# Kernel tuning notes

Hardware: AMD Instinct MI355X
Metric: run time of the kernel (lower is better)

## Reference

```python
import jax, jax.numpy as jnp
import numpy as np

B, C, H, W = 1, 256, 48, 64
HW = H * W
HIDDEN, CTX = 128, 64
LEVELS, RADIUS = 4, 4
WIN = 2 * RADIUS + 1
P = WIN * WIN                     # 81 lookup points per level
CORR_DIM = P * LEVELS             # 324
TOP_K = 3
ITERS = 4
STEP_ROT, STEP_TRANS = 0.02, 0.02


def _sample_templates():
    # 12 directions x 3 scales + identity = 37 pose perturbations (as in __init__)
    base = [([0,0,0],[1,0,0]),([0,0,0],[-1,0,0]),([0,0,0],[0,1,0]),([0,0,0],[0,-1,0]),
            ([0,0,0],[0,0,1]),([0,0,0],[0,0,-1]),([1,0,0],[0,0,0]),([-1,0,0],[0,0,0]),
            ([0,1,0],[0,0,0]),([0,-1,0],[0,0,0]),([0,0,1],[0,0,0]),([0,0,-1],[0,0,0])]
    scales = np.array([0.25, 1.0, 4.0], np.float32)
    rot = np.repeat(np.array([r for r, _ in base], np.float32), 3, axis=0)
    trs = np.repeat(np.array([t for _, t in base], np.float32), 3, axis=0)
    sc = np.tile(scales, 12)
    axes = rot / np.clip(np.linalg.norm(rot, axis=1, keepdims=True), 1e-8, None)
    ha = STEP_ROT * sc / 2.0
    dq = np.stack([np.cos(ha), axes[:, 0]*np.sin(ha), axes[:, 1]*np.sin(ha), axes[:, 2]*np.sin(ha)], -1)
    dt = trs * (STEP_TRANS * sc[:, None])
    dq = np.concatenate([dq, [[1., 0., 0., 0.]]], 0)
    dt = np.concatenate([dt, [[0., 0., 0.]]], 0)
    return jnp.asarray(dq), jnp.asarray(dt)

DQ, DT = _sample_templates()     # (37,4), (37,3)
N_SAMPLES = DQ.shape[0]


def qmul(q, r):
    w1, x1, y1, z1 = jnp.moveaxis(q, -1, 0)
    w2, x2, y2, z2 = jnp.moveaxis(r, -1, 0)
    return jnp.stack([w1*w2 - x1*x2 - y1*y2 - z1*z2,
                      w1*x2 + x1*w2 + y1*z2 - z1*y2,
                      w1*y2 - x1*z2 + y1*w2 + z1*x2,
                      w1*z2 + x1*y2 - y1*x2 + z1*w2], -1)


def qapply(q, v):
    qv = jnp.concatenate([jnp.zeros(v.shape[:-1] + (1,), v.dtype), v], -1)
    qc = q * jnp.array([1., -1., -1., -1.], q.dtype)
    return qmul(qmul(q, qv), qc)[..., 1:]


def quat_to_R(q):
    w, x, y, z = jnp.moveaxis(q, -1, 0)
    R = jnp.stack([1-2*(y*y+z*z), 2*(x*y-w*z), 2*(x*z+w*y),
                   2*(x*y+w*z), 1-2*(x*x+z*z), 2*(y*z-w*x),
                   2*(x*z-w*y), 2*(y*z+w*x), 1-2*(x*x+y*y)], -1)
    return R.reshape(q.shape[:-1] + (3, 3))


def conv3(x, w, b):
    y = jax.lax.conv_general_dilated(x, w, (1, 1), 'SAME',
                                     dimension_numbers=('NCHW', 'OIHW', 'NCHW'))
    return y + b[None, :, None, None]


def bilinear_lookup(corr_flat, Hl, Wl, x, y):
    # corr_flat: (B,HW,Hl*Wl); x,y: (B,N,HW,P) -> (B,N,HW,P), zero padding outside
    x0 = jnp.floor(x)
    y0 = jnp.floor(y)
    out = jnp.zeros(x.shape, corr_flat.dtype)
    def gather(idx):
        g = lambda ix: jnp.take_along_axis(corr_flat, ix, axis=-1)
        return jax.vmap(g, in_axes=1, out_axes=1)(idx)   # vmap over N, no corr copy
    for dx_, dy_ in ((0, 0), (1, 0), (0, 1), (1, 1)):
        xi = x0 + dx_
        yi = y0 + dy_
        wgt = (1 - jnp.abs(x - xi)) * (1 - jnp.abs(y - yi))
        valid = (xi >= 0) & (xi < Wl) & (yi >= 0) & (yi < Hl)
        idx = (jnp.clip(yi, 0, Hl - 1) * Wl + jnp.clip(xi, 0, Wl - 1)).astype(jnp.int32)
        out = out + jnp.where(valid, wgt, 0.0) * gather(idx)
    return out


def _forward(fmap_rgb, fmap_depth, depth, context, intrinsics,
             Wz, bz, Wr, br, Wq, bq, Wh, bh, Wfc, bfc):
    f32 = jnp.float32
    fx = 60. + 40. * intrinsics[:, 0]
    fy = 60. + 40. * intrinsics[:, 1]
    cx = W / 2. + 4. * (intrinsics[:, 2] - 0.5)
    cy = H / 2. + 4. * (intrinsics[:, 3] - 0.5)
    d = 4.0 + 20.0 * depth                                  # (B,H,W) metric depth

    # 4D correlation pyramid: corr[b,i,:,:] = <fmap_depth pixel i, fmap_rgb>
    fd = fmap_depth.reshape(B, C, HW).transpose(0, 2, 1)    # (B,HW,C)
    corr = jnp.einsum('bic,bchw->bihw', fd, fmap_rgb) / jnp.sqrt(f32(C))
    pyramid = []
    cl, Hl, Wl = corr, H, W
    for _ in range(LEVELS):
        pyramid.append((cl.reshape(B, HW, Hl * Wl), Hl, Wl))
        cl = cl.reshape(B, HW, Hl // 2, 2, Wl // 2, 2).mean(axis=(3, 5))
        Hl //= 2
        Wl //= 2

    # back-projected depth points (B,HW,3)
    vv, uu = jnp.meshgrid(jnp.arange(H, dtype=f32), jnp.arange(W, dtype=f32), indexing='ij')
    uu = uu.reshape(HW)
    vv = vv.reshape(HW)
    df = d.reshape(B, HW)
    X = jnp.stack([(uu[None] - cx[:, None]) / fx[:, None] * df,
                   (vv[None] - cy[:, None]) / fy[:, None] * df, df], -1)

    off = jnp.arange(-RADIUS, RADIUS + 1, dtype=f32)
    oy, ox = jnp.meshgrid(off, off, indexing='ij')
    ox = ox.reshape(P)
    oy = oy.reshape(P)

    pose = jnp.tile(jnp.array([1., 0., 0., 0., 0., 0., 0.], f32)[None, :], (B, 1))
    h = jnp.zeros((B, HIDDEN, H, W), f32)

    for _ in range(ITERS):
        qc, tc = pose[:, :4], pose[:, 4:7]
        quats = qmul(qc[:, None, :], DQ[None])              # (B,N,4)
        quats = quats / jnp.linalg.norm(quats, axis=-1, keepdims=True)
        trans = tc[:, None, :] + qapply(qc[:, None, :], DT[None])
        Rm = quat_to_R(quats)                               # (B,N,3,3)
        Xc = jnp.einsum('bnij,bpj->bnpi', Rm, X) + trans[:, :, None, :]
        z = jnp.clip(Xc[..., 2], 0.1, None)
        u = fx[:, None, None] * Xc[..., 0] / z + cx[:, None, None]   # (B,N,HW)
        v = fy[:, None, None] * Xc[..., 1] / z + cy[:, None, None]
        feats = []
        for lvl, (cfl, Hl_, Wl_) in enumerate(pyramid):
            s = f32(2 ** lvl)
            xl = u[..., None] / s + ox
            yl = v[..., None] / s + oy
            feats.append(bilinear_lookup(cfl, Hl_, Wl_, xl, yl))
        cf = jnp.concatenate(feats, -1)                     # (B,N,HW,CORR_DIM)
        conf = cf.mean(axis=(2, 3))                         # (B,N) sample confidence
        topv, topi = jax.lax.top_k(conf, TOP_K)
        wk = jax.nn.softmax(topv, axis=-1)                  # confidence-weighted top-K
        idx = jnp.broadcast_to(topi[:, :, None, None], (B, TOP_K, HW, CORR_DIM))
        sel = jnp.take_along_axis(cf, idx, axis=1)
        fused = (wk[:, :, None, None] * sel).sum(1)         # (B,HW,CORR_DIM)
        fused = fused.transpose(0, 2, 1).reshape(B, CORR_DIM, H, W)

        # ConvGRU update
        x_in = jnp.concatenate([fused, context], 1)
        hx = jnp.concatenate([h, x_in], 1)
        zg = jax.nn.sigmoid(conv3(hx, Wz, bz))
        rg = jax.nn.sigmoid(conv3(hx, Wr, br))
        qg = jnp.tanh(conv3(jnp.concatenate([rg * h, x_in], 1), Wq, bq))
        h = (1 - zg) * h + zg * qg

        # 7D pose delta head + quaternion/Lie-style update
        feat = jax.nn.relu(conv3(h, Wh, bh)).mean(axis=(2, 3))
        delta = 0.01 * (feat @ Wfc + bfc)                   # (B,7)
        dq = jnp.concatenate([1.0 + delta[:, :1], delta[:, 1:4]], -1)
        dq = dq / jnp.linalg.norm(dq, axis=-1, keepdims=True)
        tn = tc + qapply(qc, delta[:, 4:7])
        qn = qmul(qc, dq)
        qn = qn / jnp.linalg.norm(qn, axis=-1, keepdims=True)
        pose = jnp.concatenate([qn, tn], -1)
    return pose


def setup_inputs() -> dict:
    key = jax.random.key(0)
    ks = jax.random.split(key, 12)
    rn = lambda k, shape, s=1.0: s * jax.random.normal(k, shape, jnp.float32)
    Gin = HIDDEN + CORR_DIM + CTX
    sc = 1.0 / np.sqrt(Gin * 9)
    sh = 1.0 / np.sqrt(HIDDEN * 9)
    return {
        'fmap_rgb': rn(ks[0], (B, C, H, W)),
        'fmap_depth': rn(ks[1], (B, C, H, W)),
        'depth': jax.random.uniform(ks[2], (B, H, W), jnp.float32),
        'context': rn(ks[3], (B, CTX, H, W)),
        'intrinsics': jax.random.uniform(ks[4], (B, 4), jnp.float32),
        'Wz': rn(ks[5], (HIDDEN, Gin, 3, 3), sc), 'bz': jnp.zeros((HIDDEN,), jnp.float32),
        'Wr': rn(ks[6], (HIDDEN, Gin, 3, 3), sc), 'br': jnp.zeros((HIDDEN,), jnp.float32),
        'Wq': rn(ks[7], (HIDDEN, Gin, 3, 3), sc), 'bq': jnp.zeros((HIDDEN,), jnp.float32),
        'Wh': rn(ks[8], (HIDDEN, HIDDEN, 3, 3), sh), 'bh': jnp.zeros((HIDDEN,), jnp.float32),
        'Wfc': rn(ks[9], (HIDDEN, 7), 1.0 / np.sqrt(HIDDEN)), 'bfc': jnp.zeros((7,), jnp.float32),
    }


def reference(fmap_rgb, fmap_depth, depth, context, intrinsics,
              Wz, bz, Wr, br, Wq, bq, Wh, bh, Wfc, bfc):
    return _forward(fmap_rgb, fmap_depth, depth, context, intrinsics,
                    Wz, bz, Wr, br, Wq, bq, Wh, bh, Wfc, bfc)
```

## Files before the change

### kernel.cpp

```cpp
#include <hip/hip_runtime.h>
#include <math.h>

constexpr int kH = 48, kW = 64, kHW = 3072, kC = 256;
constexpr int kHidden = 128, kCtx = 64;
constexpr int kP = 81, kCorrDim = 324;
constexpr int kNS = 37, kIters = 4;
constexpr int kGin = kHidden + kCorrDim + kCtx;
constexpr int kWp2 = 66, kHp2 = 50, kPix = 3300;
constexpr int kCF = 416;
constexpr int kCHh = 128;

constexpr int kSB0 = 0, kSB1 = 4292, kSB2 = 5720, kSB3 = 6292, kSBTot = 6580;
constexpr int kHB0 = 0, kHB1 = 3552, kHB2 = 4560, kHB3 = 4872, kHBTot = 4980;

constexpr size_t U_CORR0 = 0;
constexpr size_t U_CORR1 = U_CORR0 + (size_t)kHW * 3072;
constexpr size_t U_CORR2 = U_CORR1 + (size_t)kHW * 768;
constexpr size_t U_CORR3 = U_CORR2 + (size_t)kHW * 192;
constexpr size_t U_END0  = U_CORR3 + (size_t)kHW * 48;
constexpr size_t F_X     = U_END0 / 2;
constexpr size_t F_H     = F_X + (size_t)kHW * 3;
constexpr size_t F_ZPRE  = F_H + (size_t)kHidden * kHW;
constexpr size_t F_END1  = F_ZPRE + (size_t)kHidden * kHW;
constexpr size_t U_FCT   = F_END1 * 2;
constexpr size_t U_HT    = U_FCT + (size_t)kPix * kCF;
constexpr size_t U_RHT   = U_HT + (size_t)kPix * kCHh;
constexpr size_t U_PZR   = U_RHT + (size_t)kPix * kCHh;
constexpr size_t U_PQ    = U_PZR + (size_t)16 * 9 * 17 * 512;
constexpr size_t U_PH    = U_PQ + (size_t)8 * 9 * 17 * 512;
constexpr size_t U_END2  = U_PH + (size_t)8 * 9 * 4 * 512;
constexpr size_t F_BZR   = U_END2 / 2 + 1;
constexpr size_t F_CONF  = F_BZR + 256;
constexpr size_t F_POSE  = F_CONF + 64;
constexpr size_t F_FEAT  = F_POSE + 16;
constexpr size_t F_END3  = F_FEAT + 128;
constexpr size_t U_FDT   = F_END3 * 2;
constexpr size_t U_QT    = U_FDT + (size_t)kHW * kC;
constexpr size_t U_SBOX  = U_FDT;

typedef __attribute__((ext_vector_type(8))) short short8;
typedef __attribute__((ext_vector_type(4))) float f32x4;

__device__ inline unsigned short f2b(float f) {
  unsigned int u = __float_as_uint(f);
  unsigned int r = u + 0x7FFF + ((u >> 16) & 1);
  return (unsigned short)(r >> 16);
}
__device__ inline float b2f(unsigned short u) {
  return __uint_as_float(((unsigned int)u) << 16);
}
__device__ inline int clampi(int v, int lo, int hi) { return min(max(v, lo), hi); }

__constant__ float c_rot[12][3] = {
  {0,0,0},{0,0,0},{0,0,0},{0,0,0},{0,0,0},{0,0,0},
  {1,0,0},{-1,0,0},{0,1,0},{0,-1,0},{0,0,1},{0,0,-1}};
__constant__ float c_trs[12][3] = {
  {1,0,0},{-1,0,0},{0,1,0},{0,-1,0},{0,0,1},{0,0,-1},
  {0,0,0},{0,0,0},{0,0,0},{0,0,0},{0,0,0},{0,0,0}};

__device__ inline void d_qmul(const float* q, const float* r, float* o) {
  o[0] = q[0]*r[0] - q[1]*r[1] - q[2]*r[2] - q[3]*r[3];
  o[1] = q[0]*r[1] + q[1]*r[0] + q[2]*r[3] - q[3]*r[2];
  o[2] = q[0]*r[2] - q[1]*r[3] + q[2]*r[0] + q[3]*r[1];
  o[3] = q[0]*r[3] + q[1]*r[2] - q[2]*r[1] + q[3]*r[0];
}
__device__ inline void d_qapply(const float* q, const float* v, float* o) {
  float a0 = -q[1]*v[0] - q[2]*v[1] - q[3]*v[2];
  float a1 =  q[0]*v[0] + q[2]*v[2] - q[3]*v[1];
  float a2 =  q[0]*v[1] - q[1]*v[2] + q[3]*v[0];
  float a3 =  q[0]*v[2] + q[1]*v[1] - q[2]*v[0];
  o[0] = -a0*q[1] + a1*q[0] - a2*q[3] + a3*q[2];
  o[1] = -a0*q[2] + a1*q[3] + a2*q[0] - a3*q[1];
  o[2] = -a0*q[3] - a1*q[2] + a2*q[1] + a3*q[0];
}
__device__ inline void d_intr(const float* intr, float& fx, float& fy, float& cx, float& cy) {
  fx = 60.f + 40.f*intr[0];
  fy = 60.f + 40.f*intr[1];
  cx = 32.f + 4.f*(intr[2] - 0.5f);
  cy = 24.f + 4.f*(intr[3] - 0.5f);
}
__device__ inline void sample_Rt(int t, const float* __restrict__ pose, float* S) {
  float qc[4] = {pose[0], pose[1], pose[2], pose[3]};
  float tc[3] = {pose[4], pose[5], pose[6]};
  float dq[4], dt[3];
  if (t == 36) {
    dq[0] = 1.f; dq[1] = dq[2] = dq[3] = 0.f;
    dt[0] = dt[1] = dt[2] = 0.f;
  } else {
    int j = t / 3, k = t % 3;
    float sc = (k == 0) ? 0.25f : ((k == 1) ? 1.f : 4.f);
    float rx = c_rot[j][0], ry = c_rot[j][1], rz = c_rot[j][2];
    float nrm = sqrtf(rx*rx + ry*ry + rz*rz);
    float axn = fmaxf(nrm, 1e-8f);
    float ax = rx / axn, ay = ry / axn, az = rz / axn;
    float ha = 0.02f * sc * 0.5f;
    float sh = sinf(ha), ch = cosf(ha);
    dq[0] = ch; dq[1] = ax * sh; dq[2] = ay * sh; dq[3] = az * sh;
    dt[0] = c_trs[j][0] * (0.02f * sc);
    dt[1] = c_trs[j][1] * (0.02f * sc);
    dt[2] = c_trs[j][2] * (0.02f * sc);
  }
  float qn[4];
  d_qmul(qc, dq, qn);
  float inv = 1.f / sqrtf(qn[0]*qn[0] + qn[1]*qn[1] + qn[2]*qn[2] + qn[3]*qn[3]);
  qn[0] *= inv; qn[1] *= inv; qn[2] *= inv; qn[3] *= inv;
  float tr[3];
  d_qapply(qc, dt, tr);
  float w = qn[0], x = qn[1], y = qn[2], z = qn[3];
  S[0] = 1.f - 2.f*(y*y + z*z); S[1] = 2.f*(x*y - w*z);       S[2] = 2.f*(x*z + w*y);
  S[3] = 2.f*(x*y + w*z);       S[4] = 1.f - 2.f*(x*x + z*z); S[5] = 2.f*(y*z - w*x);
  S[6] = 2.f*(x*z - w*y);       S[7] = 2.f*(y*z + w*x);       S[8] = 1.f - 2.f*(x*x + y*y);
  S[9]  = tc[0] + tr[0];
  S[10] = tc[1] + tr[1];
  S[11] = tc[2] + tr[2];
}
__device__ inline void project_uv(const float* S, const float* Xp, const float* intr,
                                  float& u, float& v) {
  float xc0 = S[0]*Xp[0] + S[1]*Xp[1] + S[2]*Xp[2] + S[9];
  float xc1 = S[3]*Xp[0] + S[4]*Xp[1] + S[5]*Xp[2] + S[10];
  float xc2 = S[6]*Xp[0] + S[7]*Xp[1] + S[8]*Xp[2] + S[11];
  float z = fmaxf(xc2, 0.1f);
  float fx, fy, cx, cy;
  d_intr(intr, fx, fy, cx, cy);
  u = fx * xc0 / z + cx;
  v = fy * xc1 / z + cy;
}

__global__ void init_k(float* __restrict__ h, unsigned int* __restrict__ zbase,
                       float* __restrict__ conf, float* __restrict__ feat,
                       float* __restrict__ pose) {
  const size_t nz = ((size_t)kPix * (kCF + 2 * kCHh)) / 2;
  for (size_t i = blockIdx.x * blockDim.x + threadIdx.x; i < nz;
       i += (size_t)gridDim.x * blockDim.x)
    zbase[i] = 0;
  int idx = blockIdx.x * blockDim.x + threadIdx.x;
  if (idx < kHidden * kHW) h[idx] = 0.f;
  if (idx < 64) conf[idx] = 0.f;
  if (idx < 128) feat[idx] = 0.f;
  if (idx == 0) {
    pose[0] = 1.f;
    for (int j = 1; j < 7; ++j) pose[j] = 0.f;
  }
}

__global__ void init2_k(const float* __restrict__ ctx, const float* __restrict__ bz,
                        const float* __restrict__ br, const float* __restrict__ depth,
                        const float* __restrict__ intr, unsigned short* __restrict__ fcT,
                        float* __restrict__ bzr, float* __restrict__ X) {
  int idx = blockIdx.x * blockDim.x + threadIdx.x;
  if (idx < kHW * 64) {
    int p = idx >> 6, c = idx & 63;
    int ppix = ((p >> 6) + 1) * kWp2 + (p & 63) + 1;
    fcT[(size_t)ppix * kCF + kCorrDim + c] = f2b(ctx[(size_t)c * kHW + p]);
  }
  if (idx < kHW) {
    float fx, fy, cx, cy;
    d_intr(intr, fx, fy, cx, cy);
    float d = 4.f + 20.f * depth[idx];
    float u = (float)(idx % kW), v = (float)(idx / kW);
    X[idx*3+0] = (u - cx) / fx * d;
    X[idx*3+1] = (v - cy) / fy * d;
    X[idx*3+2] = d;
  }
  if (idx < 256) bzr[idx] = (idx < 128) ? bz[idx] : br[idx - 128];
}

__global__ void pack_k(const float* __restrict__ W0, const float* __restrict__ W1,
                       int ocSplit, int OC, int NCH, int Cin,
                       unsigned short* __restrict__ P) {
  int idx = blockIdx.x * blockDim.x + threadIdx.x;
  int total = (OC / 16) * 9 * NCH * 64;
  if (idx >= total) return;
  int g = idx & 3;
  int m = (idx >> 2) & 15;
  int rest = idx >> 6;
  int cc = rest % NCH;
  int rest2 = rest / NCH;
  int tap = rest2 % 9;
  int ot = rest2 / 9;
  int oc = ot * 16 + m;
  union { unsigned short u[8]; uint4 q; } v;
#pragma unroll
  for (int j = 0; j < 8; ++j) {
    int ci = cc * 32 + g * 8 + j;
    float w = 0.f;
    if (ci < Cin)
      w = (oc < ocSplit) ? W0[((size_t)oc * Cin + ci) * 9 + tap]
                         : W1[((size_t)(oc - ocSplit) * Cin + ci) * 9 + tap];
    v.u[j] = f2b(w);
  }
  *(uint4*)&P[(size_t)idx * 8] = v.q;
}

__global__ __launch_bounds__(256) void t_bf16_k(const float* __restrict__ src,
                                                unsigned short* __restrict__ dst) {
  __shared__ float t[64][65];
  const int tid = threadIdx.x;
  const int p0 = blockIdx.x * 64, c0 = blockIdx.y * 64;
  const int tx = tid & 63, ty = tid >> 6;
  for (int cl = ty; cl < 64; cl += 4)
    t[cl][tx] = src[(size_t)(c0 + cl) * kHW + p0 + tx];
  __syncthreads();
  for (int pl = ty; pl < 64; pl += 4)
    dst[(size_t)(p0 + pl) * kC + c0 + tx] = f2b(t[tx][pl]);
}

__global__ __launch_bounds__(256) void corr_mfma_k(const unsigned short* __restrict__ fdT,
                                                   const unsigned short* __restrict__ qT,
                                                   unsigned short* __restrict__ Cg) {
  const int tid = threadIdx.x;
  const int wv = tid >> 6, lane = tid & 63;
  const int m = lane & 15, kg = lane >> 4;
  const int i0 = blockIdx.y * 128 + wv * 32;
  const int q0 = blockIdx.x * 128;

  f32x4 acc[2][8];
#pragma unroll
  for (int t = 0; t < 2; ++t)
#pragma unroll
    for (int u = 0; u < 8; ++u) acc[t][u] = (f32x4){0.f, 0.f, 0.f, 0.f};

#pragma unroll
  for (int kc = 0; kc < 8; ++kc) {
    const int kb = kc * 32 + kg * 8;
    short8 a[2], b[8];
#pragma unroll
    for (int t = 0; t < 2; ++t)
      a[t] = *(const short8*)&fdT[(size_t)(i0 + t * 16 + m) * kC + kb];
#pragma unroll
    for (int u = 0; u < 8; ++u)
      b[u] = *(const short8*)&qT[(size_t)(q0 + u * 16 + m) * kC + kb];
#pragma unroll
    for (int t = 0; t < 2; ++t)
#pragma unroll
      for (int u = 0; u < 8; ++u)
        acc[t][u] = __builtin_amdgcn_mfma_f32_16x16x32_bf16(a[t], b[u], acc[t][u], 0, 0, 0);
  }
  const float S = 0.0625f;
#pragma unroll
  for (int t = 0; t < 2; ++t)
#pragma unroll
    for (int u = 0; u < 8; ++u)
#pragma unroll
      for (int r = 0; r < 4; ++r)
        Cg[(size_t)(i0 + t * 16 + kg * 4 + r) * kHW + q0 + u * 16 + m] = f2b(acc[t][u][r] * S);
}

__global__ void pool2_k(const unsigned short* __restrict__ in,
                        unsigned short* __restrict__ out, int Hi, int Wi) {
  int Ho = Hi / 2, Wo = Wi / 2;
  int total = kHW * Ho * Wo;
  int idx = blockIdx.x * blockDim.x + threadIdx.x;
  if (idx >= total) return;
  int i = idx / (Ho * Wo);
  int r = idx % (Ho * Wo);
  int y = r / Wo, x = r % Wo;
  const unsigned short* p = in + (size_t)i * Hi * Wi;
  float v = 0.25f * (b2f(p[(2*y)*Wi + 2*x]) + b2f(p[(2*y)*Wi + 2*x + 1]) +
                     b2f(p[(2*y+1)*Wi + 2*x]) + b2f(p[(2*y+1)*Wi + 2*x + 1]));
  out[idx] = f2b(v);
}

template<int HL>
__device__ inline void colpref(float* base, int Wp) {
  float v[HL];
#pragma unroll
  for (int y = 0; y < HL; ++y) v[y] = base[(size_t)y * Wp];
  float run = 0.f;
#pragma unroll
  for (int y = 0; y < HL; ++y) {
    run += v[y];
    base[(size_t)y * Wp] = run;
  }
}

__global__ __launch_bounds__(256) void boxbuild_k(const unsigned short* __restrict__ corr0,
                                                  const unsigned short* __restrict__ corr1,
                                                  const unsigned short* __restrict__ corr2,
                                                  const unsigned short* __restrict__ corr3,
                                                  unsigned short* __restrict__ Sbox) {
  __shared__ float pyr[4080];
  __shared__ float hb[kHBTot];
  const int i = blockIdx.x;
  const int tid = threadIdx.x;
  const int wv = tid >> 6, lane = tid & 63;

  for (int idx = tid; idx < 4080; idx += 256) {
    float v;
    if (idx < 3072)      v = b2f(corr0[(size_t)i * 3072 + idx]);
    else if (idx < 3840) v = b2f(corr1[(size_t)i * 768 + idx - 3072]);
    else if (idx < 4032) v = b2f(corr2[(size_t)i * 192 + idx - 3840]);
    else                 v = b2f(corr3[(size_t)i * 48 + idx - 4032]);
    pyr[idx] = v;
  }
  __syncthreads();

  const int lvl_off[4] = {0, 3072, 3840, 4032};
  for (int r = wv; r < 90; r += 4) {
    int lvl, y;
    if (r < 48)      { lvl = 0; y = r; }
    else if (r < 72) { lvl = 1; y = r - 48; }
    else if (r < 84) { lvl = 2; y = r - 72; }
    else             { lvl = 3; y = r - 84; }
    const int Wl = kW >> lvl;
    float* row = &pyr[lvl_off[lvl] + y * Wl];
    float v = (lane < Wl) ? row[lane] : 0.f;
#pragma unroll
    for (int o = 1; o < 64; o <<= 1) {
      float tv = __shfl_up(v, o, 64);
      if (lane >= o) v += tv;
    }
    if (lane < Wl) row[lane] = v;
  }
  __syncthreads();

  for (int c = tid; c < 3552; c += 256) {
    int y = c / 74, as = c % 74;
    const float* pref = &pyr[y * 64];
    float Hv = 0.f;
    if (as >= 1) Hv = pref[min(63, as - 1)];
    if (as >= 10) Hv -= pref[as - 10];
    hb[kHB0 + c] = Hv;
  }
  for (int c = tid; c < 1008; c += 256) {
    int y = c / 42, as = c % 42;
    const float* pref = &pyr[3072 + y * 32];
    float Hv = 0.f;
    if (as >= 1) Hv = pref[min(31, as - 1)];
    if (as >= 10) Hv -= pref[as - 10];
    hb[kHB1 + c] = Hv;
  }
  for (int c = tid; c < 312; c += 256) {
    int y = c / 26, as = c % 26;
    const float* pref = &pyr[3840 + y * 16];
    float Hv = 0.f;
    if (as >= 1) Hv = pref[min(15, as - 1)];
    if (as >= 10) Hv -= pref[as - 10];
    hb[kHB2 + c] = Hv;
  }
  for (int c = tid; c < 108; c += 256) {
    int y = c / 18, as = c % 18;
    const float* pref = &pyr[4032 + y * 8];
    float Hv = 0.f;
    if (as >= 1) Hv = pref[min(7, as - 1)];
    if (as >= 10) Hv -= pref[as - 10];
    hb[kHB3 + c] = Hv;
  }
  __syncthreads();

  if (tid < 160) {
    if (tid < 74)       colpref<48>(hb + kHB0 + tid, 74);
    else if (tid < 116) colpref<24>(hb + kHB1 + (tid - 74), 42);
    else if (tid < 142) colpref<12>(hb + kHB2 + (tid - 116), 26);
    else                colpref<6>(hb + kHB3 + (tid - 142), 18);
  }
  __syncthreads();

  unsigned short* out = Sbox + (size_t)i * kSBTot;
  for (int c = tid; c < 4292; c += 256) {
    int bp = c / 74, as = c % 74;
    const float* col = &hb[kHB0 + as];
    float S = 0.f;
    if (bp >= 1) S = col[min(47, bp - 1) * 74];
    if (bp >= 10) S -= col[(bp - 10) * 74];
    out[kSB0 + c] = f2b(S);
  }
  for (int c = tid; c < 1428; c += 256) {
    int bp = c / 42, as = c % 42;
    const float* col = &hb[kHB1 + as];
    float S = 0.f;
    if (bp >= 1) S = col[min(23, bp - 1) * 42];
    if (bp >= 10) S -= col[(bp - 10) * 42];
    out[kSB1 + c] = f2b(S);
  }
  for (int c = tid; c < 572; c += 256) {
    int bp = c / 26, as = c % 26;
    const float* col = &hb[kHB2 + as];
    float S = 0.f;
    if (bp >= 1) S = col[min(11, bp - 1) * 26];
    if (bp >= 10) S -= col[(bp - 10) * 26];
    out[kSB2 + c] = f2b(S);
  }
  for (int c = tid; c < 288; c += 256) {
    int bp = c / 18, as = c % 18;
    const float* col = &hb[kHB3 + as];
    float S = 0.f;
    if (bp >= 1) S = col[min(5, bp - 1) * 18];
    if (bp >= 10) S -= col[(bp - 10) * 18];
    out[kSB3 + c] = f2b(S);
  }
}

__global__ __launch_bounds__(256) void conf_k(const unsigned short* __restrict__ Sbox,
                                              const float* __restrict__ X,
                                              const float* __restrict__ pose,
                                              const float* __restrict__ intr,
                                              float* __restrict__ conf) {
  const int idx = blockIdx.x * 256 + threadIdx.x;
  const int n = idx / kHW, i = idx - n * kHW;
  float S[12];
  sample_Rt(n, pose, S);
  float Xp[3] = {X[i*3], X[i*3+1], X[i*3+2]};
  float u, v;
  project_uv(S, Xp, intr, u, v);
  const unsigned short* sb = Sbox + (size_t)i * kSBTot;
  float tot = 0.f;
#pragma unroll
  for (int l = 0; l < 4; ++l) {
    const int Wp = (kW >> l) + 10, Hp = (kH >> l) + 10;
    const int so = (l == 0) ? kSB0 : (l == 1) ? kSB1 : (l == 2) ? kSB2 : kSB3;
    const float s = (float)(1 << l);
    const float bx = u / s, by = v / s;
    const float fbx = floorf(bx), fby = floorf(by);
    const int x0 = (int)fbx, y0 = (int)fby;
    const float fx = bx - fbx, fy = by - fby;
    const int xa = clampi(x0 + 5, 0, Wp - 1), xb = clampi(x0 + 6, 0, Wp - 1);
    const int ya = clampi(y0 + 5, 0, Hp - 1), yb = clampi(y0 + 6, 0, Hp - 1);
    const float s00 = b2f(sb[so + ya * Wp + xa]), s10 = b2f(sb[so + ya * Wp + xb]);
    const float s01 = b2f(sb[so + yb * Wp + xa]), s11 = b2f(sb[so + yb * Wp + xb]);
    tot += (1.f - fx) * (1.f - fy) * s00 + fx * (1.f - fy) * s10 +
           (1.f - fx) * fy * s01 + fx * fy * s11;
  }
#pragma unroll
  for (int o = 32; o; o >>= 1) tot += __shfl_xor(tot, o, 64);
  if ((threadIdx.x & 63) == 0) atomicAdd(&conf[n], tot);
}

__global__ __launch_bounds__(256) void fused_k(const unsigned short* __restrict__ corr0,
                                               const unsigned short* __restrict__ corr1,
                                               const unsigned short* __restrict__ corr2,
                                               const unsigned short* __restrict__ corr3,
                                               const float* __restrict__ X,
                                               const float* __restrict__ pose,
                                               const float* __restrict__ intr,
                                               const float* __restrict__ conf,
                                               unsigned short* __restrict__ fcT) {
  __shared__ float win[12][10][12];
  __shared__ float s_fx[12], s_fy[12];
  __shared__ int   s_ix[12], s_iy[12];
  __shared__ float s_w[3];
  __shared__ int   s_id[3];
  const int i = blockIdx.x;
  const int tid = threadIdx.x;

  if (tid == 0) {
    const float scale = 1.f / ((float)kHW * (float)kCorrDim);
    float c[kNS];
    for (int n = 0; n < kNS; ++n) c[n] = conf[n] * scale;
    int id[3] = {-1, -1, -1};
    float v[3];
    for (int k = 0; k < 3; ++k) {
      float best = -1e30f;
      int bi = -1;
      for (int n = 0; n < kNS; ++n) {
        if (n == id[0] || n == id[1] || n == id[2]) continue;
        if (c[n] > best) { best = c[n]; bi = n; }
      }
      v[k] = best;
      id[k] = bi;
    }
    float m = v[0];
    float e0 = expf(v[0] - m), e1 = expf(v[1] - m), e2 = expf(v[2] - m);
    float s = e0 + e1 + e2;
    s_w[0] = e0 / s; s_w[1] = e1 / s; s_w[2] = e2 / s;
    s_id[0] = id[0]; s_id[1] = id[1]; s_id[2] = id[2];
  }
  __syncthreads();

  if (tid < 3) {
    int n = s_id[tid];
    float S[12];
    sample_Rt(n, pose, S);
    float Xp[3] = {X[i*3], X[i*3+1], X[i*3+2]};
    float u, v;
    project_uv(S, Xp, intr, u, v);
#pragma unroll
    for (int l = 0; l < 4; ++l) {
      float s = (float)(1 << l);
      float bx = u / s, by = v / s;
      float fbx = floorf(bx), fby = floorf(by);
      s_ix[tid*4 + l] = (int)fbx;
      s_iy[tid*4 + l] = (int)fby;
      s_fx[tid*4 + l] = bx - fbx;
      s_fy[tid*4 + l] = by - fby;
    }
  }
  __syncthreads();

  for (int sidx = tid; sidx < 1200; sidx += 256) {
    const int w = sidx / 100, rem = sidx % 100;
    const int rr = rem / 10, cc = rem % 10;
    const int lvl = w & 3;
    const int Wl = kW >> lvl, Hl = kH >> lvl;
    const unsigned short* base =
        (lvl == 0) ? corr0 : (lvl == 1) ? corr1 : (lvl == 2) ? corr2 : corr3;
    const int y = s_iy[w] - 4 + rr;
    const int x = s_ix[w] - 4 + cc;
    float v = 0.f;
    if (y >= 0 && y < Hl && x >= 0 && x < Wl)
      v = b2f(base[(size_t)i * (Hl * Wl) + y * Wl + x]);
    win[w][rr][cc] = v;
  }
  __syncthreads();

  const int ppix = ((i >> 6) + 1) * kWp2 + (i & 63) + 1;
  for (int d = tid; d < kCorrDim; d += 256) {
    const int lvl = d / kP;
    const int o = d % kP;
    const int oyi = o / 9, oxi = o % 9;
    float val = 0.f;
#pragma unroll
    for (int k = 0; k < 3; ++k) {
      const int w = k * 4 + lvl;
      const float fx = s_fx[w], fy = s_fy[w];
      const float w00 = (1.f - fx) * (1.f - fy), w10 = fx * (1.f - fy);
      const float w01 = (1.f - fx) * fy, w11 = fx * fy;
      val += s_w[k] * (w00 * win[w][oyi][oxi] + w10 * win[w][oyi][oxi + 1] +
                       w01 * win[w][oyi + 1][oxi] + w11 * win[w][oyi + 1][oxi + 1]);
    }
    fcT[(size_t)ppix * kCF + d] = f2b(val);
  }
}

template<int NCHH, int NCHF>
__device__ inline void conv_core2(const unsigned short* __restrict__ srcH,
                                  const unsigned short* __restrict__ srcF,
                                  const unsigned short* __restrict__ A,
                                  int y, int xbase, int ot, int lane,
                                  f32x4 (&acc)[2]) {
  const int m = lane & 15, kg = lane >> 4;
  constexpr int NCH = NCHH + NCHF;
  const unsigned short* a_base = A + (size_t)ot * (9 * NCH * 512) + m * 32 + kg * 8;
  const int pix0 = (y + 1) * kWp2 + (xbase + 1) + m;
#pragma unroll
  for (int tap = 0; tap < 9; ++tap) {
    const int dy = tap / 3 - 1, dx = tap % 3 - 1;
    const int po = pix0 + dy * kWp2 + dx;
    const unsigned short* bh0 = srcH + (size_t)po * kCHh + kg * 8;
    const unsigned short* bf0 = srcF + (size_t)po * kCF + kg * 8;
#pragma unroll
    for (int cc = 0; cc < NCH; ++cc) {
      const int s = tap * NCH + cc;
      short8 a = *(const short8*)(a_base + (size_t)s * 512);
      short8 b0, b1;
      if (cc < NCHH) {
        b0 = *(const short8*)(bh0 + cc * 32);
        b1 = *(const short8*)(bh0 + 16 * kCHh + cc * 32);
      } else {
        b0 = *(const short8*)(bf0 + (cc - NCHH) * 32);
        b1 = *(const short8*)(bf0 + 16 * kCF + (cc - NCHH) * 32);
      }
      acc[0] = __builtin_amdgcn_mfma_f32_16x16x32_bf16(a, b0, acc[0], 0, 0, 0);
      acc[1] = __builtin_amdgcn_mfma_f32_16x16x32_bf16(a, b1, acc[1], 0, 0, 0);
    }
  }
}

__global__ __launch_bounds__(256) void conv_zr_k(const unsigned short* __restrict__ hT,
                                                 const unsigned short* __restrict__ fcT,
                                                 const unsigned short* __restrict__ P,
                                                 const float* __restrict__ bzr,
                                                 float* __restrict__ zpre,
                                                 const float* __restrict__ hbuf,
                                                 unsigned short* __restrict__ rhT) {
  const int tid = threadIdx.x;
  const int wv = tid >> 6, lane = tid & 63;
  const int y = blockIdx.y >> 1, xbase = (blockIdx.y & 1) * 32;
  const int ot = blockIdx.x * 4 + wv;
  f32x4 acc[2] = {{0.f,0.f,0.f,0.f},{0.f,0.f,0.f,0.f}};
  conv_core2<4, 13>(hT, fcT, P, y, xbase, ot, lane, acc);
  const int m = lane & 15, kg = lane >> 4;
#pragma unroll
  for (int t = 0; t < 2; ++t)
#pragma unroll
    for (int r = 0; r < 4; ++r) {
      const int oc = ot * 16 + kg * 4 + r;
      const int pxx = xbase + t * 16 + m;
      const int px = y * kW + pxx;
      const float val = acc[t][r] + bzr[oc];
      if (oc < kHidden) {
        zpre[(size_t)oc * kHW + px] = val;
      } else {
        const float rg = 1.f / (1.f + expf(-val));
        const int ppix = (y + 1) * kWp2 + pxx + 1;
        rhT[(size_t)ppix * kCHh + oc - kHidden] =
            f2b(rg * hbuf[(size_t)(oc - kHidden) * kHW + px]);
      }
    }
}

__global__ __launch_bounds__(256) void conv_q_k(const unsigned short* __restrict__ rhT,
                                                const unsigned short* __restrict__ fcT,
                                                unsigned short* __restrict__ hT,
                                                const unsigned short* __restrict__ P,
                                                const float* __restrict__ bq,
                                                const float* __restrict__ zpre,
                                                float* __restrict__ hbuf) {
  const int tid = threadIdx.x;
  const int wv = tid >> 6, lane = tid & 63;
  const int y = blockIdx.y >> 1, xbase = (blockIdx.y & 1) * 32;
  const int ot = blockIdx.x * 4 + wv;
  f32x4 acc[2] = {{0.f,0.f,0.f,0.f},{0.f,0.f,0.f,0.f}};
  conv_core2<4, 13>(rhT, fcT, P, y, xbase, ot, lane, acc);
  const int m = lane & 15, kg = lane >> 4;
#pragma unroll
  for (int t = 0; t < 2; ++t)
#pragma unroll
    for (int r = 0; r < 4; ++r) {
      const int oc = ot * 16 + kg * 4 + r;
      const int pxx = xbase + t * 16 + m;
      const int px = y * kW + pxx;
      const size_t off = (size_t)oc * kHW + px;
      const float q = acc[t][r] + bq[oc];
      const float zg = 1.f / (1.f + expf(-zpre[off]));
      const float hn = (1.f - zg) * hbuf[off] + zg * tanhf(q);
      hbuf[off] = hn;
      const int ppix = (y + 1) * kWp2 + pxx + 1;
      hT[(size_t)ppix * kCHh + oc] = f2b(hn);
    }
}

__global__ __launch_bounds__(256) void conv_h_k(const unsigned short* __restrict__ hT,
                                                const unsigned short* __restrict__ P,
                                                const float* __restrict__ bh,
                                                float* __restrict__ feat) {
  const int tid = threadIdx.x;
  const int wv = tid >> 6, lane = tid & 63;
  const int y = blockIdx.y >> 1, xbase = (blockIdx.y & 1) * 32;
  const int ot = blockIdx.x * 4 + wv;
  f32x4 acc[2] = {{0.f,0.f,0.f,0.f},{0.f,0.f,0.f,0.f}};
  conv_core2<4, 0>(hT, hT, P, y, xbase, ot, lane, acc);
  const int m = lane & 15, kg = lane >> 4;
#pragma unroll
  for (int r = 0; r < 4; ++r) {
    const int oc = ot * 16 + kg * 4 + r;
    const float bv = bh[oc];
    float v = fmaxf(acc[0][r] + bv, 0.f) + fmaxf(acc[1][r] + bv, 0.f);
    v += __shfl_xor(v, 1, 64);
    v += __shfl_xor(v, 2, 64);
    v += __shfl_xor(v, 4, 64);
    v += __shfl_xor(v, 8, 64);
    if (m == 0) atomicAdd(&feat[oc], v);
  }
}

__global__ void pose_update_k(float* __restrict__ feat, float* __restrict__ conf,
                              const float* __restrict__ Wfc,
                              const float* __restrict__ bfc, float* __restrict__ pose,
                              float* __restrict__ out) {
  __shared__ float s_d[7];
  int t = threadIdx.x;
  if (t < 7) {
    float s = 0.f;
    const float inv = 1.f / (float)kHW;
    for (int k = 0; k < kHidden; ++k) s += (feat[k] * inv) * Wfc[k * 7 + t];
    s_d[t] = 0.01f * (s + bfc[t]);
  }
  __syncthreads();
  if (t < kHidden) feat[t] = 0.f;
  if (t < 64) conf[t] = 0.f;
  if (t != 0) return;
  float qc[4] = {pose[0], pose[1], pose[2], pose[3]};
  float tc[3] = {pose[4], pose[5], pose[6]};
  float dq[4] = {1.f + s_d[0], s_d[1], s_d[2], s_d[3]};
  float inv = 1.f / sqrtf(dq[0]*dq[0] + dq[1]*dq[1] + dq[2]*dq[2] + dq[3]*dq[3]);
  dq[0] *= inv; dq[1] *= inv; dq[2] *= inv; dq[3] *= inv;
  float dv[3] = {s_d[4], s_d[5], s_d[6]};
  float rv[3];
  d_qapply(qc, dv, rv);
  float tn[3] = {tc[0] + rv[0], tc[1] + rv[1], tc[2] + rv[2]};
  float qn[4];
  d_qmul(qc, dq, qn);
  float inv2 = 1.f / sqrtf(qn[0]*qn[0] + qn[1]*qn[1] + qn[2]*qn[2] + qn[3]*qn[3]);
  qn[0] *= inv2; qn[1] *= inv2; qn[2] *= inv2; qn[3] *= inv2;
  pose[0] = qn[0]; pose[1] = qn[1]; pose[2] = qn[2]; pose[3] = qn[3];
  pose[4] = tn[0]; pose[5] = tn[1]; pose[6] = tn[2];
  out[0] = qn[0]; out[1] = qn[1]; out[2] = qn[2]; out[3] = qn[3];
  out[4] = tn[0]; out[5] = tn[1]; out[6] = tn[2];
}

extern "C" void kernel_launch(void* const* d_in, const int* in_sizes, int n_in,
                              void* d_out, int out_size, void* d_ws, size_t ws_size,
                              hipStream_t stream) {
  const float* frgb  = (const float*)d_in[0];
  const float* fdep  = (const float*)d_in[1];
  const float* depth = (const float*)d_in[2];
  const float* ctx   = (const float*)d_in[3];
  const float* intr  = (const float*)d_in[4];
  const float* Wz = (const float*)d_in[5];
  const float* bz = (const float*)d_in[6];
  const float* Wr = (const float*)d_in[7];
  const float* br = (const float*)d_in[8];
  const float* Wq = (const float*)d_in[9];
  const float* bq = (const float*)d_in[10];
  const float* Wh = (const float*)d_in[11];
  const float* bh = (const float*)d_in[12];
  const float* Wfc = (const float*)d_in[13];
  const float* bfc = (const float*)d_in[14];
  float* outp = (float*)d_out;

  float* ws = (float*)d_ws;
  unsigned short* us = (unsigned short*)d_ws;
  unsigned short* corr0 = us + U_CORR0;
  unsigned short* corr1 = us + U_CORR1;
  unsigned short* corr2 = us + U_CORR2;
  unsigned short* corr3 = us + U_CORR3;
  float* X    = ws + F_X;
  float* hbuf = ws + F_H;
  float* zpre = ws + F_ZPRE;
  unsigned short* fcT = us + U_FCT;
  unsigned short* hT  = us + U_HT;
  unsigned short* rhT = us + U_RHT;
  unsigned short* Pzr = us + U_PZR;
  unsigned short* Pq  = us + U_PQ;
  unsigned short* Ph  = us + U_PH;
  float* bzr  = ws + F_BZR;
  float* conf = ws + F_CONF;
  float* pose = ws + F_POSE;
  float* feat = ws + F_FEAT;
  unsigned short* fdT  = us + U_FDT;
  unsigned short* qT   = us + U_QT;
  unsigned short* Sbox = us + U_SBOX;

  init_k<<<1536, 256, 0, stream>>>(hbuf, (unsigned int*)fcT, conf, feat, pose);
  init2_k<<<768, 256, 0, stream>>>(ctx, bz, br, depth, intr, fcT, bzr, X);
  pack_k<<<(16 * 9 * 17 * 64 + 255) / 256, 256, 0, stream>>>(Wz, Wr, 128, 256, 17,
                                                             kGin, Pzr);
  pack_k<<<(8 * 9 * 17 * 64 + 255) / 256, 256, 0, stream>>>(Wq, Wq, 128, 128, 17,
                                                            kGin, Pq);
  pack_k<<<(8 * 9 * 4 * 64 + 255) / 256, 256, 0, stream>>>(Wh, Wh, 128, 128, 4,
                                                           kHidden, Ph);
  t_bf16_k<<<dim3(48, 4), 256, 0, stream>>>(fdep, fdT);
  t_bf16_k<<<dim3(48, 4), 256, 0, stream>>>(frgb, qT);
  corr_mfma_k<<<dim3(24, 24), 256, 0, stream>>>(fdT, qT, corr0);
  {
    int t1 = kHW * 24 * 32, t2 = kHW * 12 * 16, t3 = kHW * 6 * 8;
    pool2_k<<<(t1 + 255) / 256, 256, 0, stream>>>(corr0, corr1, 48, 64);
    pool2_k<<<(t2 + 255) / 256, 256, 0, stream>>>(corr1, corr2, 24, 32);
    pool2_k<<<(t3 + 255) / 256, 256, 0, stream>>>(corr2, corr3, 12, 16);
  }
  boxbuild_k<<<kHW, 256, 0, stream>>>(corr0, corr1, corr2, corr3, Sbox);

  for (int it = 0; it < kIters; ++it) {
    conf_k<<<444, 256, 0, stream>>>(Sbox, X, pose, intr, conf);
    fused_k<<<kHW, 256, 0, stream>>>(corr0, corr1, corr2, corr3, X, pose, intr,
                                     conf, fcT);
    conv_zr_k<<<dim3(4, 96), 256, 0, stream>>>(hT, fcT, Pzr, bzr, zpre, hbuf, rhT);
    conv_q_k<<<dim3(2, 96), 256, 0, stream>>>(rhT, fcT, hT, Pq, bq, zpre, hbuf);
    conv_h_k<<<dim3(2, 96), 256, 0, stream>>>(hT, Ph, bh, feat);
    pose_update_k<<<1, 128, 0, stream>>>(feat, conf, Wfc, bfc, pose, outp);
  }
}
```

Measured before the change: 875.5 us.

## Fuse pyramid pooling into boxbuild, merge init kernels, halve conv pixel tiles

The three pool2 launches are removed, and boxbuild now builds corr1-3 in shared memory from corr0 and writes them back to global memory. The init kernels are reorganised: the scalar init moves into init_k and the context transpose gets its own initctx_k. The GRU conv kernels now cover 16 pixels per wave instead of 32, which doubles the grid to raise parallelism at the cost of less reuse of the weight fragments. Together these target launch overhead, redundant global reads of the pyramid, and low occupancy in the conv stage.

```diff
diff --git a/kernel.cpp b/kernel.cpp
--- a/kernel.cpp
+++ b/kernel.cpp
@@ -126,7 +126,11 @@
   v = fy * xc1 / z + cy;
 }
 
-__global__ void init_k(float* __restrict__ h, unsigned int* __restrict__ zbase,
+__global__ void init_k(const float* __restrict__ ctx, const float* __restrict__ bz,
+                       const float* __restrict__ br, const float* __restrict__ depth,
+                       const float* __restrict__ intr, float* __restrict__ h,
+                       unsigned int* __restrict__ zbase, unsigned short* __restrict__ fcT,
+                       float* __restrict__ bzr, float* __restrict__ X,
                        float* __restrict__ conf, float* __restrict__ feat,
                        float* __restrict__ pose) {
   const size_t nz = ((size_t)kPix * (kCF + 2 * kCHh)) / 2;
@@ -135,24 +139,6 @@
     zbase[i] = 0;
   int idx = blockIdx.x * blockDim.x + threadIdx.x;
   if (idx < kHidden * kHW) h[idx] = 0.f;
-  if (idx < 64) conf[idx] = 0.f;
-  if (idx < 128) feat[idx] = 0.f;
-  if (idx == 0) {
-    pose[0] = 1.f;
-    for (int j = 1; j < 7; ++j) pose[j] = 0.f;
-  }
-}
-
-__global__ void init2_k(const float* __restrict__ ctx, const float* __restrict__ bz,
-                        const float* __restrict__ br, const float* __restrict__ depth,
-                        const float* __restrict__ intr, unsigned short* __restrict__ fcT,
-                        float* __restrict__ bzr, float* __restrict__ X) {
-  int idx = blockIdx.x * blockDim.x + threadIdx.x;
-  if (idx < kHW * 64) {
-    int p = idx >> 6, c = idx & 63;
-    int ppix = ((p >> 6) + 1) * kWp2 + (p & 63) + 1;
-    fcT[(size_t)ppix * kCF + kCorrDim + c] = f2b(ctx[(size_t)c * kHW + p]);
-  }
   if (idx < kHW) {
     float fx, fy, cx, cy;
     d_intr(intr, fx, fy, cx, cy);
@@ -163,6 +149,20 @@
     X[idx*3+2] = d;
   }
   if (idx < 256) bzr[idx] = (idx < 128) ? bz[idx] : br[idx - 128];
+  if (idx < 64) conf[idx] = 0.f;
+  if (idx < 128) feat[idx] = 0.f;
+  if (idx == 0) {
+    pose[0] = 1.f;
+    for (int j = 1; j < 7; ++j) pose[j] = 0.f;
+  }
+}
+__global__ void initctx_k(const float* __restrict__ ctx, unsigned short* __restrict__ fcT) {
+  int idx = blockIdx.x * blockDim.x + threadIdx.x;
+  if (idx < kHW * 64) {
+    int p = idx >> 6, c = idx & 63;
+    int ppix = ((p >> 6) + 1) * kWp2 + (p & 63) + 1;
+    fcT[(size_t)ppix * kCF + kCorrDim + c] = f2b(ctx[(size_t)c * kHW + p]);
+  }
 }
 
 __global__ void pack_k(const float* __restrict__ W0, const float* __restrict__ W1,
@@ -246,21 +246,6 @@
         Cg[(size_t)(i0 + t * 16 + kg * 4 + r) * kHW + q0 + u * 16 + m] = f2b(acc[t][u][r] * S);
 }
 
-__global__ void pool2_k(const unsigned short* __restrict__ in,
-                        unsigned short* __restrict__ out, int Hi, int Wi) {
-  int Ho = Hi / 2, Wo = Wi / 2;
-  int total = kHW * Ho * Wo;
-  int idx = blockIdx.x * blockDim.x + threadIdx.x;
-  if (idx >= total) return;
-  int i = idx / (Ho * Wo);
-  int r = idx % (Ho * Wo);
-  int y = r / Wo, x = r % Wo;
-  const unsigned short* p = in + (size_t)i * Hi * Wi;
-  float v = 0.25f * (b2f(p[(2*y)*Wi + 2*x]) + b2f(p[(2*y)*Wi + 2*x + 1]) +
-                     b2f(p[(2*y+1)*Wi + 2*x]) + b2f(p[(2*y+1)*Wi + 2*x + 1]));
-  out[idx] = f2b(v);
-}
-
 template<int HL>
 __device__ inline void colpref(float* base, int Wp) {
   float v[HL];
@@ -275,9 +260,9 @@
 }
 
 __global__ __launch_bounds__(256) void boxbuild_k(const unsigned short* __restrict__ corr0,
-                                                  const unsigned short* __restrict__ corr1,
-                                                  const unsigned short* __restrict__ corr2,
-                                                  const unsigned short* __restrict__ corr3,
+                                                  unsigned short* __restrict__ corr1,
+                                                  unsigned short* __restrict__ corr2,
+                                                  unsigned short* __restrict__ corr3,
                                                   unsigned short* __restrict__ Sbox) {
   __shared__ float pyr[4080];
   __shared__ float hb[kHBTot];
@@ -285,13 +270,37 @@
   const int tid = threadIdx.x;
   const int wv = tid >> 6, lane = tid & 63;
 
-  for (int idx = tid; idx < 4080; idx += 256) {
-    float v;
-    if (idx < 3072)      v = b2f(corr0[(size_t)i * 3072 + idx]);
-    else if (idx < 3840) v = b2f(corr1[(size_t)i * 768 + idx - 3072]);
-    else if (idx < 4032) v = b2f(corr2[(size_t)i * 192 + idx - 3840]);
-    else                 v = b2f(corr3[(size_t)i * 48 + idx - 4032]);
-    pyr[idx] = v;
+  for (int idx = tid; idx < 3072; idx += 256)
+    pyr[idx] = b2f(corr0[(size_t)i * 3072 + idx]);
+  __syncthreads();
+
+  for (int c = tid; c < 768; c += 256) {
+    int y = c >> 5, x = c & 31;
+    float v = 0.25f * (pyr[(2*y)*64 + 2*x] + pyr[(2*y)*64 + 2*x + 1] +
+                       pyr[(2*y+1)*64 + 2*x] + pyr[(2*y+1)*64 + 2*x + 1]);
+    unsigned short b = f2b(v);
+    corr1[(size_t)i * 768 + c] = b;
+    pyr[3072 + c] = b2f(b);
+  }
+  __syncthreads();
+  for (int c = tid; c < 192; c += 256) {
+    int y = c >> 4, x = c & 15;
+    const float* p = pyr + 3072;
+    float v = 0.25f * (p[(2*y)*32 + 2*x] + p[(2*y)*32 + 2*x + 1] +
+                       p[(2*y+1)*32 + 2*x] + p[(2*y+1)*32 + 2*x + 1]);
+    unsigned short b = f2b(v);
+    corr2[(size_t)i * 192 + c] = b;
+    pyr[3840 + c] = b2f(b);
+  }
+  __syncthreads();
+  for (int c = tid; c < 48; c += 256) {
+    int y = c >> 3, x = c & 7;
+    const float* p = pyr + 3840;
+    float v = 0.25f * (p[(2*y)*16 + 2*x] + p[(2*y)*16 + 2*x + 1] +
+                       p[(2*y+1)*16 + 2*x] + p[(2*y+1)*16 + 2*x + 1]);
+    unsigned short b = f2b(v);
+    corr3[(size_t)i * 48 + c] = b;
+    pyr[4032 + c] = b2f(b);
   }
   __syncthreads();
 
@@ -523,11 +532,11 @@
 }
 
 template<int NCHH, int NCHF>
-__device__ inline void conv_core2(const unsigned short* __restrict__ srcH,
-                                  const unsigned short* __restrict__ srcF,
-                                  const unsigned short* __restrict__ A,
-                                  int y, int xbase, int ot, int lane,
-                                  f32x4 (&acc)[2]) {
+__device__ inline void conv_core16(const unsigned short* __restrict__ srcH,
+                                   const unsigned short* __restrict__ srcF,
+                                   const unsigned short* __restrict__ A,
+                                   int y, int xbase, int ot, int lane,
+                                   f32x4& acc) {
   const int m = lane & 15, kg = lane >> 4;
   constexpr int NCH = NCHH + NCHF;
   const unsigned short* a_base = A + (size_t)ot * (9 * NCH * 512) + m * 32 + kg * 8;
@@ -542,16 +551,9 @@
     for (int cc = 0; cc < NCH; ++cc) {
       const int s = tap * NCH + cc;
       short8 a = *(const short8*)(a_base + (size_t)s * 512);
-      short8 b0, b1;
-      if (cc < NCHH) {
-        b0 = *(const short8*)(bh0 + cc * 32);
-        b1 = *(const short8*)(bh0 + 16 * kCHh + cc * 32);
-      } else {
-        b0 = *(const short8*)(bf0 + (cc - NCHH) * 32);
-        b1 = *(const short8*)(bf0 + 16 * kCF + (cc - NCHH) * 32);
-      }
-      acc[0] = __builtin_amdgcn_mfma_f32_16x16x32_bf16(a, b0, acc[0], 0, 0, 0);
-      acc[1] = __builtin_amdgcn_mfma_f32_16x16x32_bf16(a, b1, acc[1], 0, 0, 0);
+      short8 b = (cc < NCHH) ? *(const short8*)(bh0 + cc * 32)
+                             : *(const short8*)(bf0 + (cc - NCHH) * 32);
+      acc = __builtin_amdgcn_mfma_f32_16x16x32_bf16(a, b, acc, 0, 0, 0);
     }
   }
 }
@@ -565,28 +567,26 @@
                                                  unsigned short* __restrict__ rhT) {
   const int tid = threadIdx.x;
   const int wv = tid >> 6, lane = tid & 63;
-  const int y = blockIdx.y >> 1, xbase = (blockIdx.y & 1) * 32;
+  const int y = blockIdx.y >> 2, xbase = (blockIdx.y & 3) * 16;
   const int ot = blockIdx.x * 4 + wv;
-  f32x4 acc[2] = {{0.f,0.f,0.f,0.f},{0.f,0.f,0.f,0.f}};
-  conv_core2<4, 13>(hT, fcT, P, y, xbase, ot, lane, acc);
+  f32x4 acc = {0.f, 0.f, 0.f, 0.f};
+  conv_core16<4, 13>(hT, fcT, P, y, xbase, ot, lane, acc);
   const int m = lane & 15, kg = lane >> 4;
 #pragma unroll
-  for (int t = 0; t < 2; ++t)
-#pragma unroll
-    for (int r = 0; r < 4; ++r) {
-      const int oc = ot * 16 + kg * 4 + r;
-      const int pxx = xbase + t * 16 + m;
-      const int px = y * kW + pxx;
-      const float val = acc[t][r] + bzr[oc];
-      if (oc < kHidden) {
-        zpre[(size_t)oc * kHW + px] = val;
-      } else {
-        const float rg = 1.f / (1.f + expf(-val));
-        const int ppix = (y + 1) * kWp2 + pxx + 1;
-        rhT[(size_t)ppix * kCHh + oc - kHidden] =
-            f2b(rg * hbuf[(size_t)(oc - kHidden) * kHW + px]);
-      }
+  for (int r = 0; r < 4; ++r) {
+    const int oc = ot * 16 + kg * 4 + r;
+    const int pxx = xbase + m;
+    const int px = y * kW + pxx;
+    const float val = acc[r] + bzr[oc];
+    if (oc < kHidden) {
+      zpre[(size_t)oc * kHW + px] = val;
+    } else {
+      const float rg = 1.f / (1.f + expf(-val));
+      const int ppix = (y + 1) * kWp2 + pxx + 1;
+      rhT[(size_t)ppix * kCHh + oc - kHidden] =
+          f2b(rg * hbuf[(size_t)(oc - kHidden) * kHW + px]);
     }
+  }
 }
 
 __global__ __launch_bounds__(256) void conv_q_k(const unsigned short* __restrict__ rhT,
@@ -598,26 +598,24 @@
                                                 float* __restrict__ hbuf) {
   const int tid = threadIdx.x;
   const int wv = tid >> 6, lane = tid & 63;
-  const int y = blockIdx.y >> 1, xbase = (blockIdx.y & 1) * 32;
+  const int y = blockIdx.y >> 2, xbase = (blockIdx.y & 3) * 16;
   const int ot = blockIdx.x * 4 + wv;
-  f32x4 acc[2] = {{0.f,0.f,0.f,0.f},{0.f,0.f,0.f,0.f}};
-  conv_core2<4, 13>(rhT, fcT, P, y, xbase, ot, lane, acc);
+  f32x4 acc = {0.f, 0.f, 0.f, 0.f};
+  conv_core16<4, 13>(rhT, fcT, P, y, xbase, ot, lane, acc);
   const int m = lane & 15, kg = lane >> 4;
 #pragma unroll
-  for (int t = 0; t < 2; ++t)
-#pragma unroll
-    for (int r = 0; r < 4; ++r) {
-      const int oc = ot * 16 + kg * 4 + r;
-      const int pxx = xbase + t * 16 + m;
-      const int px = y * kW + pxx;
-      const size_t off = (size_t)oc * kHW + px;
-      const float q = acc[t][r] + bq[oc];
-      const float zg = 1.f / (1.f + expf(-zpre[off]));
-      const float hn = (1.f - zg) * hbuf[off] + zg * tanhf(q);
-      hbuf[off] = hn;
-      const int ppix = (y + 1) * kWp2 + pxx + 1;
-      hT[(size_t)ppix * kCHh + oc] = f2b(hn);
-    }
+  for (int r = 0; r < 4; ++r) {
+    const int oc = ot * 16 + kg * 4 + r;
+    const int pxx = xbase + m;
+    const int px = y * kW + pxx;
+    const size_t off = (size_t)oc * kHW + px;
+    const float q = acc[r] + bq[oc];
+    const float zg = 1.f / (1.f + expf(-zpre[off]));
+    const float hn = (1.f - zg) * hbuf[off] + zg * tanhf(q);
+    hbuf[off] = hn;
+    const int ppix = (y + 1) * kWp2 + pxx + 1;
+    hT[(size_t)ppix * kCHh + oc] = f2b(hn);
+  }
 }
 
 __global__ __launch_bounds__(256) void conv_h_k(const unsigned short* __restrict__ hT,
@@ -626,16 +624,15 @@
                                                 float* __restrict__ feat) {
   const int tid = threadIdx.x;
   const int wv = tid >> 6, lane = tid & 63;
-  const int y = blockIdx.y >> 1, xbase = (blockIdx.y & 1) * 32;
+  const int y = blockIdx.y >> 2, xbase = (blockIdx.y & 3) * 16;
   const int ot = blockIdx.x * 4 + wv;
-  f32x4 acc[2] = {{0.f,0.f,0.f,0.f},{0.f,0.f,0.f,0.f}};
-  conv_core2<4, 0>(hT, hT, P, y, xbase, ot, lane, acc);
+  f32x4 acc = {0.f, 0.f, 0.f, 0.f};
+  conv_core16<4, 0>(hT, hT, P, y, xbase, ot, lane, acc);
   const int m = lane & 15, kg = lane >> 4;
 #pragma unroll
   for (int r = 0; r < 4; ++r) {
     const int oc = ot * 16 + kg * 4 + r;
-    const float bv = bh[oc];
-    float v = fmaxf(acc[0][r] + bv, 0.f) + fmaxf(acc[1][r] + bv, 0.f);
+    float v = fmaxf(acc[r] + bh[oc], 0.f);
     v += __shfl_xor(v, 1, 64);
     v += __shfl_xor(v, 2, 64);
     v += __shfl_xor(v, 4, 64);
@@ -722,8 +719,9 @@
   unsigned short* qT   = us + U_QT;
   unsigned short* Sbox = us + U_SBOX;
 
-  init_k<<<1536, 256, 0, stream>>>(hbuf, (unsigned int*)fcT, conf, feat, pose);
-  init2_k<<<768, 256, 0, stream>>>(ctx, bz, br, depth, intr, fcT, bzr, X);
+  init_k<<<1536, 256, 0, stream>>>(ctx, bz, br, depth, intr, hbuf,
+                                   (unsigned int*)fcT, fcT, bzr, X, conf, feat, pose);
+  initctx_k<<<768, 256, 0, stream>>>(ctx, fcT);
   pack_k<<<(16 * 9 * 17 * 64 + 255) / 256, 256, 0, stream>>>(Wz, Wr, 128, 256, 17,
                                                              kGin, Pzr);
   pack_k<<<(8 * 9 * 17 * 64 + 255) / 256, 256, 0, stream>>>(Wq, Wq, 128, 128, 17,
@@ -733,21 +731,15 @@
   t_bf16_k<<<dim3(48, 4), 256, 0, stream>>>(fdep, fdT);
   t_bf16_k<<<dim3(48, 4), 256, 0, stream>>>(frgb, qT);
   corr_mfma_k<<<dim3(24, 24), 256, 0, stream>>>(fdT, qT, corr0);
-  {
-    int t1 = kHW * 24 * 32, t2 = kHW * 12 * 16, t3 = kHW * 6 * 8;
-    pool2_k<<<(t1 + 255) / 256, 256, 0, stream>>>(corr0, corr1, 48, 64);
-    pool2_k<<<(t2 + 255) / 256, 256, 0, stream>>>(corr1, corr2, 24, 32);
-    pool2_k<<<(t3 + 255) / 256, 256, 0, stream>>>(corr2, corr3, 12, 16);
-  }
   boxbuild_k<<<kHW, 256, 0, stream>>>(corr0, corr1, corr2, corr3, Sbox);
 
   for (int it = 0; it < kIters; ++it) {
     conf_k<<<444, 256, 0, stream>>>(Sbox, X, pose, intr, conf);
     fused_k<<<kHW, 256, 0, stream>>>(corr0, corr1, corr2, corr3, X, pose, intr,
                                      conf, fcT);
-    conv_zr_k<<<dim3(4, 96), 256, 0, stream>>>(hT, fcT, Pzr, bzr, zpre, hbuf, rhT);
-    conv_q_k<<<dim3(2, 96), 256, 0, stream>>>(rhT, fcT, hT, Pq, bq, zpre, hbuf);
-    conv_h_k<<<dim3(2, 96), 256, 0, stream>>>(hT, Ph, bh, feat);
+    conv_zr_k<<<dim3(4, 192), 256, 0, stream>>>(hT, fcT, Pzr, bzr, zpre, hbuf, rhT);
+    conv_q_k<<<dim3(2, 192), 256, 0, stream>>>(rhT, fcT, hT, Pq, bq, zpre, hbuf);
+    conv_h_k<<<dim3(2, 192), 256, 0, stream>>>(hT, Ph, bh, feat);
     pose_update_k<<<1, 128, 0, stream>>>(feat, conf, Wfc, bfc, pose, outp);
   }
 }
```

New measurement: 917.4 us. 1.05x slower.
